# Kernel optimization log

Hardware: AMD Instinct MI355X
Metric: run time of the kernel (lower is better)

## Reference

```python
import jax, jax.numpy as jnp
import numpy as np

WINDOW_SIZE = 128  # matches init_kwargs


def setup_inputs() -> dict:
    key = jax.random.key(0)
    kq, kk, kv = jax.random.split(key, 3)
    B, H, S, D = 1, 8, 2048, 64
    q = jax.random.normal(kq, (B, H, S, D), dtype=jnp.float32)
    k = jax.random.normal(kk, (B, H, S, D), dtype=jnp.float32)
    v = jax.random.normal(kv, (B, H, S, D), dtype=jnp.float32)
    return {"q": q, "k": k, "v": v}


def reference(q, k, v):
    # q, k, v: [B, H, S, D]
    B, H, S, D = q.shape
    w = WINDOW_SIZE // 2  # half-window = 64
    offs = jnp.arange(-w, w + 1)                      # [W] with W = 2w+1 = 129
    pos = jnp.arange(S)[:, None] + offs[None, :]      # [S, W] absolute key index per query
    valid = (pos >= 0) & (pos < S)                    # edge clipping: start=max(0,i-w), end=min(S,i+w+1)
    pos_c = jnp.clip(pos, 0, S - 1)

    # Gather banded keys/values: [B, H, S, W, D]
    k_win = k[:, :, pos_c, :]
    v_win = v[:, :, pos_c, :]

    scale = 1.0 / jnp.sqrt(jnp.asarray(D, dtype=q.dtype))
    scores = jnp.einsum('bhsd,bhswd->bhsw', q, k_win) * scale  # [B, H, S, W]
    neg_inf = jnp.asarray(-jnp.inf, dtype=scores.dtype)
    scores = jnp.where(valid[None, None, :, :], scores, neg_inf)

    attn = jax.nn.softmax(scores, axis=-1)            # every row has >= w+1 valid entries, no NaNs
    out = jnp.einsum('bhsw,bhswd->bhsd', attn, v_win) # [B, H, S, D]
    return out
```

## Files before the change

kernel.cpp:

```cpp
#include <hip/hip_runtime.h>
#include <hip/hip_fp16.h>


#define SEQ 2048
#define NH 8
#define QB 64
#define ROWS 192
#define KSTR 72
#define PSTR 40

typedef _Float16 f16x8 __attribute__((ext_vector_type(8)));
typedef float    f32x4 __attribute__((ext_vector_type(4)));

static __device__ __forceinline__ ushort4 pack4(float4 f, float s) {
    union { _Float16 h[4]; ushort4 u; } p;
    p.h[0] = (_Float16)(f.x * s);
    p.h[1] = (_Float16)(f.y * s);
    p.h[2] = (_Float16)(f.z * s);
    p.h[3] = (_Float16)(f.w * s);
    return p.u;
}

__global__ __launch_bounds__(512) void local_attn(
    const float* __restrict__ q,
    const float* __restrict__ k,
    const float* __restrict__ v,
    float* __restrict__ out)
{
    __shared__ __align__(16) _Float16      Kl[ROWS * KSTR];
    __shared__ __align__(16) unsigned char VtB[64 * 384];
    __shared__ __align__(16) _Float16      Pm[8][16 * PSTR];
    __shared__ __align__(16) float         Cmb[4][64][20];

    const int tid  = threadIdx.x;
    const int lane = tid & 63;
    const int w    = tid >> 6;
    const int t    = w & 3;
    const int half = w >> 2;
    const int l15  = lane & 15;
    const int l4   = lane >> 4;
    const int bx   = blockIdx.x;
    const int h     = bx & 7;
    const int qbase = (bx >> 3) * QB;

    const float* kh = k + (size_t)h * SEQ * 64;
    const float* vh = v + (size_t)h * SEQ * 64;
    const float* qh = q + (size_t)h * SEQ * 64;

    const float* qrow = qh + (size_t)(qbase + t * 16 + l15) * 64 + l4 * 8;
    float4 q0 = *(const float4*)(qrow);
    float4 q1 = *(const float4*)(qrow + 4);
    float4 q2 = *(const float4*)(qrow + 32);
    float4 q3 = *(const float4*)(qrow + 36);
    union uf { f16x8 v; _Float16 hh[8]; };
    uf A0, A1;
    A0.hh[0] = (_Float16)(q0.x * 0.125f); A0.hh[1] = (_Float16)(q0.y * 0.125f);
    A0.hh[2] = (_Float16)(q0.z * 0.125f); A0.hh[3] = (_Float16)(q0.w * 0.125f);
    A0.hh[4] = (_Float16)(q1.x * 0.125f); A0.hh[5] = (_Float16)(q1.y * 0.125f);
    A0.hh[6] = (_Float16)(q1.z * 0.125f); A0.hh[7] = (_Float16)(q1.w * 0.125f);
    A1.hh[0] = (_Float16)(q2.x * 0.125f); A1.hh[1] = (_Float16)(q2.y * 0.125f);
    A1.hh[2] = (_Float16)(q2.z * 0.125f); A1.hh[3] = (_Float16)(q2.w * 0.125f);
    A1.hh[4] = (_Float16)(q3.x * 0.125f); A1.hh[5] = (_Float16)(q3.y * 0.125f);
    A1.hh[6] = (_Float16)(q3.z * 0.125f); A1.hh[7] = (_Float16)(q3.w * 0.125f);

    {
        const int d4  = (tid & 15) << 2;
        const int lr0 = tid >> 4;
        #pragma unroll
        for (int it = 0; it < 6; ++it) {
            const int lr = lr0 + it * 32;
            const int g  = qbase - 64 + lr;
            float4 kv4 = make_float4(0.f, 0.f, 0.f, 0.f);
            float4 vv4 = make_float4(0.f, 0.f, 0.f, 0.f);
            if (g >= 0 && g < SEQ) {
                kv4 = *(const float4*)(kh + (size_t)g * 64 + d4);
                vv4 = *(const float4*)(vh + (size_t)g * 64 + d4);
            }
            *(ushort4*)&Kl[lr * KSTR + d4] = pack4(kv4, 1.0f);
            float vs[4] = {vv4.x, vv4.y, vv4.z, vv4.w};
            #pragma unroll
            for (int i2 = 0; i2 < 4; ++i2) {
                int d = d4 + i2;
                int u = (lr >> 3) ^ (d & 7);
                *(_Float16*)&VtB[d * 384 + (u << 4) + (lr & 7) * 2] = (_Float16)vs[i2];
            }
        }
    }
    __syncthreads();

    _Float16* Pw = Pm[w];
    float rsum[4] = {0.f, 0.f, 0.f, 0.f};
    f32x4 o[4];
    #pragma unroll
    for (int dt = 0; dt < 4; ++dt) o[dt] = (f32x4){0.f, 0.f, 0.f, 0.f};

    #pragma unroll
    for (int c = 0; c < 3; ++c) {
        const int r0 = (half * 3 + c) * 32;

        #pragma unroll
        for (int t2 = 0; t2 < 2; ++t2) {
            const int r = r0 + t2 * 16 + l15;
            f16x8 b0 = *(const f16x8*)&Kl[r * KSTR + l4 * 8];
            f16x8 b1 = *(const f16x8*)&Kl[r * KSTR + 32 + l4 * 8];
            f32x4 cacc = {0.f, 0.f, 0.f, 0.f};
            cacc = __builtin_amdgcn_mfma_f32_16x16x32_f16(A0.v, b0, cacc, 0, 0, 0);
            cacc = __builtin_amdgcn_mfma_f32_16x16x32_f16(A1.v, b1, cacc, 0, 0, 0);
            const int g  = qbase - 64 + r;
            const bool gv = (g >= 0) & (g < SEQ);
            #pragma unroll
            for (int j = 0; j < 4; ++j) {
                const int qg = qbase + t * 16 + l4 * 4 + j;
                const bool valid = gv && (g >= qg - 64) && (g <= qg + 64);
                const float e = valid ? __expf(cacc[j]) : 0.f;
                rsum[j] += e;
                Pw[(l4 * 4 + j) * PSTR + t2 * 16 + l15] = (_Float16)e;
            }
        }

        asm volatile("s_waitcnt lgkmcnt(0)" ::: "memory");

        f16x8 a = *(const f16x8*)&Pw[l15 * PSTR + l4 * 8];
        #pragma unroll
        for (int dt = 0; dt < 4; ++dt) {
            const int dim = dt * 16 + l15;
            const int u   = ((r0 + l4 * 8) >> 3) ^ (dim & 7);
            f16x8 bb = *(const f16x8*)&VtB[dim * 384 + (u << 4)];
            o[dt] = __builtin_amdgcn_mfma_f32_16x16x32_f16(a, bb, o[dt], 0, 0, 0);
        }
    }

    if (half == 1) {
        #pragma unroll
        for (int dt = 0; dt < 4; ++dt)
            *(f32x4*)&Cmb[t][lane][dt * 4] = o[dt];
        f32x4 pr = {rsum[0], rsum[1], rsum[2], rsum[3]};
        *(f32x4*)&Cmb[t][lane][16] = pr;
    }
    __syncthreads();
    if (half == 0) {
        #pragma unroll
        for (int dt = 0; dt < 4; ++dt) {
            f32x4 p = *(const f32x4*)&Cmb[t][lane][dt * 4];
            o[dt] += p;
        }
        f32x4 pr = *(const f32x4*)&Cmb[t][lane][16];

        #pragma unroll
        for (int j = 0; j < 4; ++j) {
            float l = rsum[j] + pr[j];
            l += __shfl_xor(l, 1, 64);
            l += __shfl_xor(l, 2, 64);
            l += __shfl_xor(l, 4, 64);
            l += __shfl_xor(l, 8, 64);
            const float inv = 1.0f / l;
            const int qg = qbase + t * 16 + l4 * 4 + j;
            #pragma unroll
            for (int dt = 0; dt < 4; ++dt)
                out[((size_t)h * SEQ + qg) * 64 + dt * 16 + l15] = o[dt][j] * inv;
        }
    }
}

extern "C" void kernel_launch(void* const* d_in, const int* in_sizes, int n_in,
                              void* d_out, int out_size, void* d_ws, size_t ws_size,
                              hipStream_t stream)
{
    const float* q = (const float*)d_in[0];
    const float* k = (const float*)d_in[1];
    const float* v = (const float*)d_in[2];
    float* out = (float*)d_out;

    local_attn<<<256, 512, 0, stream>>>(q, k, v, out);
}
```

Baseline: 11.81 us.

## Load K directly into registers and defer V transpose to overlap with QK

K tiles are now loaded straight from global memory into registers in MFMA operand layout, so the K shared-memory staging buffer goes away. V is prefetched into registers at kernel start, and its transposed write to shared memory is deferred until after the QK^T and exp phase, so the global V latency overlaps with compute. P tiles get per-chunk buffers so that all score chunks can be computed before the single barrier. This removes one shared-memory round-trip and moves the barrier later, at the cost of much higher register pressure (96 extra floats for K) and redundant K loads across the four waves that share a half.

```diff
diff --git a/kernel.cpp b/kernel.cpp
--- a/kernel.cpp
+++ b/kernel.cpp
@@ -3,23 +3,11 @@
 
 
 #define SEQ 2048
-#define NH 8
 #define QB 64
-#define ROWS 192
-#define KSTR 72
 #define PSTR 40
 
 typedef _Float16 f16x8 __attribute__((ext_vector_type(8)));
 typedef float    f32x4 __attribute__((ext_vector_type(4)));
-
-static __device__ __forceinline__ ushort4 pack4(float4 f, float s) {
-    union { _Float16 h[4]; ushort4 u; } p;
-    p.h[0] = (_Float16)(f.x * s);
-    p.h[1] = (_Float16)(f.y * s);
-    p.h[2] = (_Float16)(f.z * s);
-    p.h[3] = (_Float16)(f.w * s);
-    return p.u;
-}
 
 __global__ __launch_bounds__(512) void local_attn(
     const float* __restrict__ q,
@@ -27,9 +15,8 @@
     const float* __restrict__ v,
     float* __restrict__ out)
 {
-    __shared__ __align__(16) _Float16      Kl[ROWS * KSTR];
     __shared__ __align__(16) unsigned char VtB[64 * 384];
-    __shared__ __align__(16) _Float16      Pm[8][16 * PSTR];
+    __shared__ __align__(16) _Float16      Pm[24][16 * PSTR];
     __shared__ __align__(16) float         Cmb[4][64][20];
 
     const int tid  = threadIdx.x;
@@ -43,15 +30,42 @@
     const int h     = bx & 7;
     const int qbase = (bx >> 3) * QB;
 
+    const float* qh = q + (size_t)h * SEQ * 64;
     const float* kh = k + (size_t)h * SEQ * 64;
     const float* vh = v + (size_t)h * SEQ * 64;
-    const float* qh = q + (size_t)h * SEQ * 64;
+
+    const int d4  = (tid & 15) << 2;
+    const int vr0 = tid >> 4;
+    float4 vreg[6];
+    #pragma unroll
+    for (int it = 0; it < 6; ++it) {
+        int g = qbase - 64 + vr0 + it * 32;
+        g = g < 0 ? 0 : (g > SEQ - 1 ? SEQ - 1 : g);
+        vreg[it] = *(const float4*)(vh + (size_t)g * 64 + d4);
+    }
 
     const float* qrow = qh + (size_t)(qbase + t * 16 + l15) * 64 + l4 * 8;
     float4 q0 = *(const float4*)(qrow);
     float4 q1 = *(const float4*)(qrow + 4);
     float4 q2 = *(const float4*)(qrow + 32);
     float4 q3 = *(const float4*)(qrow + 36);
+
+    float4 kreg[3][2][4];
+    #pragma unroll
+    for (int c = 0; c < 3; ++c) {
+        #pragma unroll
+        for (int t2 = 0; t2 < 2; ++t2) {
+            const int r = (half * 3 + c) * 32 + t2 * 16 + l15;
+            int g = qbase - 64 + r;
+            g = g < 0 ? 0 : (g > SEQ - 1 ? SEQ - 1 : g);
+            const float* kr = kh + (size_t)g * 64 + l4 * 8;
+            kreg[c][t2][0] = *(const float4*)(kr);
+            kreg[c][t2][1] = *(const float4*)(kr + 4);
+            kreg[c][t2][2] = *(const float4*)(kr + 32);
+            kreg[c][t2][3] = *(const float4*)(kr + 36);
+        }
+    }
+
     union uf { f16x8 v; _Float16 hh[8]; };
     uf A0, A1;
     A0.hh[0] = (_Float16)(q0.x * 0.125f); A0.hh[1] = (_Float16)(q0.y * 0.125f);
@@ -63,49 +77,24 @@
     A1.hh[4] = (_Float16)(q3.x * 0.125f); A1.hh[5] = (_Float16)(q3.y * 0.125f);
     A1.hh[6] = (_Float16)(q3.z * 0.125f); A1.hh[7] = (_Float16)(q3.w * 0.125f);
 
-    {
-        const int d4  = (tid & 15) << 2;
-        const int lr0 = tid >> 4;
-        #pragma unroll
-        for (int it = 0; it < 6; ++it) {
-            const int lr = lr0 + it * 32;
-            const int g  = qbase - 64 + lr;
-            float4 kv4 = make_float4(0.f, 0.f, 0.f, 0.f);
-            float4 vv4 = make_float4(0.f, 0.f, 0.f, 0.f);
-            if (g >= 0 && g < SEQ) {
-                kv4 = *(const float4*)(kh + (size_t)g * 64 + d4);
-                vv4 = *(const float4*)(vh + (size_t)g * 64 + d4);
-            }
-            *(ushort4*)&Kl[lr * KSTR + d4] = pack4(kv4, 1.0f);
-            float vs[4] = {vv4.x, vv4.y, vv4.z, vv4.w};
-            #pragma unroll
-            for (int i2 = 0; i2 < 4; ++i2) {
-                int d = d4 + i2;
-                int u = (lr >> 3) ^ (d & 7);
-                *(_Float16*)&VtB[d * 384 + (u << 4) + (lr & 7) * 2] = (_Float16)vs[i2];
-            }
-        }
-    }
-    __syncthreads();
-
-    _Float16* Pw = Pm[w];
     float rsum[4] = {0.f, 0.f, 0.f, 0.f};
-    f32x4 o[4];
-    #pragma unroll
-    for (int dt = 0; dt < 4; ++dt) o[dt] = (f32x4){0.f, 0.f, 0.f, 0.f};
-
     #pragma unroll
     for (int c = 0; c < 3; ++c) {
-        const int r0 = (half * 3 + c) * 32;
-
+        _Float16* Pw = Pm[w * 3 + c];
         #pragma unroll
         for (int t2 = 0; t2 < 2; ++t2) {
-            const int r = r0 + t2 * 16 + l15;
-            f16x8 b0 = *(const f16x8*)&Kl[r * KSTR + l4 * 8];
-            f16x8 b1 = *(const f16x8*)&Kl[r * KSTR + 32 + l4 * 8];
+            const int r = (half * 3 + c) * 32 + t2 * 16 + l15;
+            uf b0, b1;
+            #pragma unroll
+            for (int j = 0; j < 4; ++j) {
+                b0.hh[j]     = (_Float16)kreg[c][t2][0][j];
+                b0.hh[j + 4] = (_Float16)kreg[c][t2][1][j];
+                b1.hh[j]     = (_Float16)kreg[c][t2][2][j];
+                b1.hh[j + 4] = (_Float16)kreg[c][t2][3][j];
+            }
             f32x4 cacc = {0.f, 0.f, 0.f, 0.f};
-            cacc = __builtin_amdgcn_mfma_f32_16x16x32_f16(A0.v, b0, cacc, 0, 0, 0);
-            cacc = __builtin_amdgcn_mfma_f32_16x16x32_f16(A1.v, b1, cacc, 0, 0, 0);
+            cacc = __builtin_amdgcn_mfma_f32_16x16x32_f16(A0.v, b0.v, cacc, 0, 0, 0);
+            cacc = __builtin_amdgcn_mfma_f32_16x16x32_f16(A1.v, b1.v, cacc, 0, 0, 0);
             const int g  = qbase - 64 + r;
             const bool gv = (g >= 0) & (g < SEQ);
             #pragma unroll
@@ -117,10 +106,28 @@
                 Pw[(l4 * 4 + j) * PSTR + t2 * 16 + l15] = (_Float16)e;
             }
         }
+    }
 
-        asm volatile("s_waitcnt lgkmcnt(0)" ::: "memory");
+    #pragma unroll
+    for (int it = 0; it < 6; ++it) {
+        const int r = vr0 + it * 32;
+        #pragma unroll
+        for (int i2 = 0; i2 < 4; ++i2) {
+            const int d = d4 + i2;
+            const int u = (r >> 3) ^ (d & 7);
+            *(_Float16*)&VtB[d * 384 + (u << 4) + (r & 7) * 2] =
+                (_Float16)vreg[it][i2];
+        }
+    }
+    __syncthreads();
 
-        f16x8 a = *(const f16x8*)&Pw[l15 * PSTR + l4 * 8];
+    f32x4 o[4];
+    #pragma unroll
+    for (int dt = 0; dt < 4; ++dt) o[dt] = (f32x4){0.f, 0.f, 0.f, 0.f};
+    #pragma unroll
+    for (int c = 0; c < 3; ++c) {
+        const int r0 = (half * 3 + c) * 32;
+        f16x8 a = *(const f16x8*)&Pm[w * 3 + c][l15 * PSTR + l4 * 8];
         #pragma unroll
         for (int dt = 0; dt < 4; ++dt) {
             const int dim = dt * 16 + l15;
```

After: 15.20 us. 1.29x slower.
